# Optimization experiments

Measured on AMD Instinct MI355X. Metric: run time of the kernel, lower is better.

## Reference

```python
import jax, jax.numpy as jnp
import numpy as np

N = 8192      # batch*seq_len (batch=4, seq_len=2048)
DK = 256
DV = 256


def setup_inputs() -> dict:
    key = jax.random.key(0)
    ks = jax.random.split(key, 9)
    s = 1.0 / np.sqrt(DK)
    return {
        "q": jax.random.normal(ks[0], (N, DK), jnp.float32),
        "k": jax.random.normal(ks[1], (N, DK), jnp.float32),
        "v": jax.random.normal(ks[2], (N, DV), jnp.float32),
        "Wq": jax.random.normal(ks[3], (DK, DK), jnp.float32) * s,
        "bq": jnp.zeros((DK,), jnp.float32),
        "Wk": jax.random.normal(ks[4], (DK, DK), jnp.float32) * s,
        "bk": jnp.zeros((DK,), jnp.float32),
        "Wv": jax.random.normal(ks[5], (DV, DV), jnp.float32) * s,
        "bv": jnp.zeros((DV,), jnp.float32),
        "seq_len": 2048,
    }


def reference(q, k, v, Wq, bq, Wk, bk, Wv, bv, seq_len):
    # torch Linear: y = x @ W.T + b
    Q = q @ Wq.T + bq                       # [N, dk]
    K = k @ Wk.T + bk                       # [N, dk]
    V = v @ Wv.T + bv                       # [N, dv]
    sqrt_dk = jnp.sqrt(jnp.asarray(DK, Q.dtype))
    score = (Q @ K.T) / sqrt_dk             # [N, N] — attends over ALL tokens
    # original reshapes to (B, S, N) and softmaxes over dim=-1, which is
    # identical to row-wise softmax on the [N, N] score matrix
    attn = jax.nn.softmax(score, axis=-1)   # [N, N]
    return attn @ V                          # [N, dv]
```

## Files before the change

kernel.cpp:

```cpp
#include <hip/hip_runtime.h>
#include <hip/hip_bf16.h>


typedef __attribute__((ext_vector_type(8))) short short8;
typedef __attribute__((ext_vector_type(4))) short short4v;
typedef __attribute__((ext_vector_type(4))) float f32x4;
typedef __attribute__((ext_vector_type(4))) float float4v;
typedef __attribute__((ext_vector_type(16))) float f32x16;

#define MFMA16 __builtin_amdgcn_mfma_f32_16x16x32_bf16
#define MFMA32 __builtin_amdgcn_mfma_f32_32x32x16_bf16

namespace {
constexpr int kN = 8192;
constexpr int kD = 256;
constexpr int kKVB = 32;
}

__device__ __forceinline__ unsigned short f2bf(float x) {
  union { float f; unsigned u; } v; v.f = x;
  unsigned r = v.u + 0x7FFFu + ((v.u >> 16) & 1u);
  return (unsigned short)(r >> 16);
}

__device__ __forceinline__ unsigned cvtpk_bf16(float lo, float hi) {
  unsigned d;
  asm("v_cvt_pk_bf16_f32 %0, %1, %2" : "=v"(d) : "v"(lo), "v"(hi));
  return d;
}

__device__ __forceinline__ void gll16(const short* g, short* lp) {
  __builtin_amdgcn_global_load_lds(
      (const __attribute__((address_space(1))) void*)g,
      (__attribute__((address_space(3))) void*)lp, 16, 0, 0);
}

__global__ __launch_bounds__(256) void proj_kernel(
    const float* __restrict__ qx, const float* __restrict__ kx, const float* __restrict__ vx,
    const float* __restrict__ Wq, const float* __restrict__ bq,
    const float* __restrict__ Wk, const float* __restrict__ bk,
    const float* __restrict__ Wv, const float* __restrict__ bv,
    short* __restrict__ Qimg, short* __restrict__ Kimg, short* __restrict__ Vimg)
{
  const int mode = blockIdx.z;
  const float* X; const float* W; const float* B;
  if (mode == 0)      { X = qx; W = Wq; B = bq; }
  else if (mode == 1) { X = kx; W = Wk; B = bk; }
  else                { X = vx; W = Wv; B = bv; }

  const int nb = blockIdx.x * 64;
  const int ob = blockIdx.y * 64;

  __shared__ short XA[64][264];
  __shared__ short WB[64][264];

  const int t  = threadIdx.x;
  {
    const int c4 = t & 63;
    const int r0 = t >> 6;
#pragma unroll
    for (int p = 0; p < 16; ++p) {
      const int r = p * 4 + r0;
      float4v xv = *(const float4v*)(X + (size_t)(nb + r) * kD + c4 * 4);
      float4v wv = *(const float4v*)(W + (size_t)(ob + r) * kD + c4 * 4);
      short4v xs, wsv;
#pragma unroll
      for (int j = 0; j < 4; ++j) { xs[j] = (short)f2bf(xv[j]); wsv[j] = (short)f2bf(wv[j]); }
      *(short4v*)(&XA[r][c4 * 4]) = xs;
      *(short4v*)(&WB[r][c4 * 4]) = wsv;
    }
  }
  __syncthreads();

  const int w  = t >> 6;
  const int l  = t & 63;
  const int lr = l & 15;
  const int g  = l >> 4;

  const f32x4 vzero = {0.f, 0.f, 0.f, 0.f};
  f32x4 acc[4];
#pragma unroll
  for (int ct = 0; ct < 4; ++ct) acc[ct] = vzero;

#pragma unroll
  for (int s = 0; s < 8; ++s) {
    short8 af = *(const short8*)(&XA[w * 16 + lr][s * 32 + g * 8]);
#pragma unroll
    for (int ct = 0; ct < 4; ++ct) {
      short8 bf = *(const short8*)(&WB[ct * 16 + lr][s * 32 + g * 8]);
      acc[ct] = MFMA16(af, bf, acc[ct], 0, 0, 0);
    }
  }

#pragma unroll
  for (int ct = 0; ct < 4; ++ct) {
    const int o = ob + ct * 16 + lr;
    const float bias = B[o];
    if (mode == 2) {
      const int n0 = nb + w * 16 + g * 4;
      short4v vs;
#pragma unroll
      for (int r2 = 0; r2 < 4; ++r2) vs[r2] = (short)f2bf(acc[ct][r2] + bias);
      const size_t idx = (size_t)(n0 >> 5) * 8192 + (size_t)(o >> 5) * 1024
                       + (size_t)((n0 >> 4) & 1) * 512 + (size_t)((n0 >> 3) & 1) * 256
                       + (size_t)(o & 31) * 8 + (n0 & 7);
      *(short4v*)(Vimg + idx) = vs;
    } else {
      short* Out = (mode == 0) ? Qimg : Kimg;
      const float sc = (mode == 0) ? 0.0625f : 1.0f;
#pragma unroll
      for (int r2 = 0; r2 < 4; ++r2) {
        const int n = nb + w * 16 + g * 4 + r2;
        const size_t idx = (size_t)(n >> 5) * 8192 + (size_t)(o >> 4) * 512
                         + (size_t)((o >> 3) & 1) * 256 + (size_t)(n & 31) * 8 + (o & 7);
        Out[idx] = (short)f2bf((acc[ct][r2] + bias) * sc);
      }
    }
  }
}

template<int SPLIT>
__global__ __launch_bounds__(512) void flash_kernel(
    const short* __restrict__ Qimg, const short* __restrict__ Kimg, const short* __restrict__ Vimg,
    float* __restrict__ Op, float2* __restrict__ Ml)
{
  constexpr int kIters = (kN / SPLIT) / kKVB;
  const int linear = (int)blockIdx.x;
  int sp, qb;
  if (SPLIT == 8) { sp = linear & 7; qb = linear >> 3; }
  else { const int xcd = linear & 7; sp = xcd >> 1; qb = ((linear >> 3) << 1) | (xcd & 1); }
  const int kvblk0 = sp * (kN / SPLIT / 32);

  __shared__ short sbuf[2][2][8192];

  const int t = threadIdx.x;
  const int w = t >> 6, l = t & 63;
  const int hf = l >> 5;
  const int lc = l & 31;

  {
    const short* kg = Kimg + (size_t)kvblk0 * 8192 + w * 512 + l * 8;
    const short* vg = Vimg + (size_t)kvblk0 * 8192 + w * 512 + l * 8;
    gll16(kg,        &sbuf[0][0][w * 512]);
    gll16(kg + 4096, &sbuf[0][0][4096 + w * 512]);
    gll16(vg,        &sbuf[0][1][w * 512]);
    gll16(vg + 4096, &sbuf[0][1][4096 + w * 512]);
  }

  short8 qf[16];
  {
    const short* qsrc = Qimg + (size_t)(qb * 8 + w) * 8192 + l * 8;
#pragma unroll
    for (int ks = 0; ks < 16; ++ks) qf[ks] = *(const short8*)(qsrc + ks * 512);
  }

  f32x16 oacc[8];
#pragma unroll
  for (int dvt = 0; dvt < 8; ++dvt)
#pragma unroll
    for (int r = 0; r < 16; ++r) oacc[dvt][r] = 0.f;
  float mr = -1e30f, lsum = 0.f;

  asm volatile("s_waitcnt vmcnt(0)" ::: "memory");
  __syncthreads();

  for (int it = 0; it < kIters; ++it) {
    const int cur = it & 1;
    if (it + 1 < kIters) {
      const short* kg = Kimg + (size_t)(kvblk0 + it + 1) * 8192 + w * 512 + l * 8;
      const short* vg = Vimg + (size_t)(kvblk0 + it + 1) * 8192 + w * 512 + l * 8;
      short* kb = &sbuf[cur ^ 1][0][0];
      short* vb = &sbuf[cur ^ 1][1][0];
      gll16(kg,        kb + w * 512);
      gll16(kg + 4096, kb + 4096 + w * 512);
      gll16(vg,        vb + w * 512);
      gll16(vg + 4096, vb + 4096 + w * 512);
    }

    f32x16 sacc;
#pragma unroll
    for (int r = 0; r < 16; ++r) sacc[r] = 0.f;
    __builtin_amdgcn_s_setprio(1);
#pragma unroll
    for (int ks = 0; ks < 16; ++ks) {
      short8 kf = *(const short8*)(&sbuf[cur][0][ks * 512 + l * 8]);
      sacc = MFMA32(kf, qf[ks], sacc, 0, 0, 0);
    }
    __builtin_amdgcn_s_setprio(0);

    float pmax = sacc[0];
#pragma unroll
    for (int r = 1; r < 16; ++r) pmax = fmaxf(pmax, sacc[r]);
    pmax = fmaxf(pmax, __shfl_xor(pmax, 32));
    const bool noskip = !__all(pmax - mr <= 8.f);
    if (noskip) {
      const float newm = fmaxf(mr, pmax);
      const float corr = __expf(mr - newm);
      mr = newm;
      lsum *= corr;
#pragma unroll
      for (int r = 0; r < 16; ++r) {
        const float c = __shfl(corr, (r & 3) + 8 * (r >> 2) + 4 * hf);
#pragma unroll
        for (int dvt = 0; dvt < 8; ++dvt) oacc[dvt][r] *= c;
      }
    }
    float psum = 0.f;
#pragma unroll
    for (int r = 0; r < 16; ++r) { sacc[r] = __expf(sacc[r] - mr); psum += sacc[r]; }
    psum += __shfl_xor(psum, 32);
    lsum += psum;

    short8 pa[2];
#pragma unroll
    for (int w2 = 0; w2 < 2; ++w2) {
      const int b = w2 * 8;
      const unsigned A0 = cvtpk_bf16(sacc[b + 0], sacc[b + 1]);
      const unsigned A1 = cvtpk_bf16(sacc[b + 2], sacc[b + 3]);
      const unsigned B0 = cvtpk_bf16(sacc[b + 4], sacc[b + 5]);
      const unsigned B1 = cvtpk_bf16(sacc[b + 6], sacc[b + 7]);
      const unsigned sA0 = (unsigned)__shfl_xor((int)A0, 32);
      const unsigned sA1 = (unsigned)__shfl_xor((int)A1, 32);
      const unsigned sB0 = (unsigned)__shfl_xor((int)B0, 32);
      const unsigned sB1 = (unsigned)__shfl_xor((int)B1, 32);
      union { unsigned u[4]; short8 s; } pu;
      pu.u[0] = hf ? sB0 : A0;
      pu.u[1] = hf ? sB1 : A1;
      pu.u[2] = hf ? B0 : sA0;
      pu.u[3] = hf ? B1 : sA1;
      pa[w2] = pu.s;
    }

    __builtin_amdgcn_s_setprio(1);
#pragma unroll
    for (int dvt = 0; dvt < 8; ++dvt) {
#pragma unroll
      for (int ks2 = 0; ks2 < 2; ++ks2) {
        short8 vf = *(const short8*)(&sbuf[cur][1][(dvt * 2 + ks2) * 512 + l * 8]);
        oacc[dvt] = MFMA32(pa[ks2], vf, oacc[dvt], 0, 0, 0);
      }
    }
    __builtin_amdgcn_s_setprio(0);

    asm volatile("s_waitcnt vmcnt(0)" ::: "memory");
    __syncthreads();
  }

  const int qrow0 = qb * 256 + w * 32;
#pragma unroll
  for (int dvt = 0; dvt < 8; ++dvt)
#pragma unroll
    for (int r = 0; r < 16; ++r) {
      const int q = qrow0 + (r & 3) + 8 * (r >> 2) + 4 * hf;
      Op[((size_t)sp * kN + q) * kD + dvt * 32 + lc] = oacc[dvt][r];
    }
  if (l < 32) Ml[(size_t)sp * kN + qrow0 + l] = make_float2(mr, lsum);
}

template<int SPLIT>
__global__ __launch_bounds__(256) void merge_kernel(
    const float* __restrict__ Op, const float2* __restrict__ Ml, float* __restrict__ out)
{
  const int qrow = blockIdx.x;
  const int d = threadIdx.x;
  float m[SPLIT], li[SPLIT];
  float M = -1e30f;
#pragma unroll
  for (int s = 0; s < SPLIT; ++s) {
    const float2 a = Ml[(size_t)s * kN + qrow];
    m[s] = a.x; li[s] = a.y;
    M = fmaxf(M, m[s]);
  }
  float L = 0.f, accv = 0.f;
#pragma unroll
  for (int s = 0; s < SPLIT; ++s) {
    const float wgt = __expf(m[s] - M);
    L += wgt * li[s];
    accv += wgt * Op[((size_t)s * kN + qrow) * kD + d];
  }
  out[(size_t)qrow * kD + d] = accv / L;
}

extern "C" void kernel_launch(void* const* d_in, const int* in_sizes, int n_in,
                              void* d_out, int out_size, void* d_ws, size_t ws_size,
                              hipStream_t stream)
{
  const float* q  = (const float*)d_in[0];
  const float* k  = (const float*)d_in[1];
  const float* v  = (const float*)d_in[2];
  const float* Wq = (const float*)d_in[3];
  const float* bq = (const float*)d_in[4];
  const float* Wk = (const float*)d_in[5];
  const float* bk = (const float*)d_in[6];
  const float* Wv = (const float*)d_in[7];
  const float* bv = (const float*)d_in[8];

  char* ws = (char*)d_ws;
  short* Qimg = (short*)(ws);
  short* Kimg = (short*)(ws + ((size_t)4 << 20));
  short* Vimg = (short*)(ws + ((size_t)8 << 20));
  const size_t opOff = (size_t)12 << 20;
  float* Op = (float*)(ws + opOff);

  proj_kernel<<<dim3(kN / 64, kD / 64, 3), 256, 0, stream>>>(
      q, k, v, Wq, bq, Wk, bk, Wv, bv, Qimg, Kimg, Vimg);

  const size_t opBytes8 = (size_t)8 * kN * kD * 4;
  const size_t need8 = opOff + opBytes8 + (size_t)8 * kN * 8;
  if (ws_size >= need8) {
    float2* Ml = (float2*)(ws + opOff + opBytes8);
    flash_kernel<8><<<dim3(256), 512, 0, stream>>>(Qimg, Kimg, Vimg, Op, Ml);
    merge_kernel<8><<<dim3(kN), 256, 0, stream>>>(Op, Ml, (float*)d_out);
  } else {
    const size_t opBytes4 = (size_t)4 * kN * kD * 4;
    float2* Ml = (float2*)(ws + opOff + opBytes4);
    flash_kernel<4><<<dim3(128), 512, 0, stream>>>(Qimg, Kimg, Vimg, Op, Ml);
    merge_kernel<4><<<dim3(kN), 256, 0, stream>>>(Op, Ml, (float*)d_out);
  }
}
```

Before: 112.4 us.

## Shrink flash blocks to 4 waves, reuse X across output tiles, interleave softmax with PV

The flash kernel now runs 256-thread blocks covering 128 query rows, twice as many blocks, with launch bounds requesting two blocks per CU. The KV tile load is restructured to use all 256 threads. The exp/convert/PV path is split into two halves so the second half of the exponentials can overlap the first half's MFMAs. The projection kernel now loads each X tile once and loops over all four W output tiles, and Q/K use a transposed MFMA so their stores become 4-wide vectors. The risks are register pressure under the two-blocks-per-CU bound and a different pattern of KV tile reuse across blocks.

```diff
diff --git a/kernel.cpp b/kernel.cpp
--- a/kernel.cpp
+++ b/kernel.cpp
@@ -35,92 +35,114 @@
       (__attribute__((address_space(3))) void*)lp, 16, 0, 0);
 }
 
-__global__ __launch_bounds__(256) void proj_kernel(
+__global__ __launch_bounds__(256, 2) void proj_kernel(
     const float* __restrict__ qx, const float* __restrict__ kx, const float* __restrict__ vx,
     const float* __restrict__ Wq, const float* __restrict__ bq,
     const float* __restrict__ Wk, const float* __restrict__ bk,
     const float* __restrict__ Wv, const float* __restrict__ bv,
     short* __restrict__ Qimg, short* __restrict__ Kimg, short* __restrict__ Vimg)
 {
-  const int mode = blockIdx.z;
+  const int mode = blockIdx.y;
   const float* X; const float* W; const float* B;
   if (mode == 0)      { X = qx; W = Wq; B = bq; }
   else if (mode == 1) { X = kx; W = Wk; B = bk; }
   else                { X = vx; W = Wv; B = bv; }
 
   const int nb = blockIdx.x * 64;
-  const int ob = blockIdx.y * 64;
 
   __shared__ short XA[64][264];
   __shared__ short WB[64][264];
 
   const int t  = threadIdx.x;
-  {
-    const int c4 = t & 63;
-    const int r0 = t >> 6;
-#pragma unroll
-    for (int p = 0; p < 16; ++p) {
-      const int r = p * 4 + r0;
-      float4v xv = *(const float4v*)(X + (size_t)(nb + r) * kD + c4 * 4);
-      float4v wv = *(const float4v*)(W + (size_t)(ob + r) * kD + c4 * 4);
-      short4v xs, wsv;
-#pragma unroll
-      for (int j = 0; j < 4; ++j) { xs[j] = (short)f2bf(xv[j]); wsv[j] = (short)f2bf(wv[j]); }
-      *(short4v*)(&XA[r][c4 * 4]) = xs;
-      *(short4v*)(&WB[r][c4 * 4]) = wsv;
-    }
-  }
-  __syncthreads();
+  const int c4 = t & 63;
+  const int r0 = t >> 6;
+
+#pragma unroll
+  for (int p = 0; p < 16; ++p) {
+    const int r = p * 4 + r0;
+    float4v xv = *(const float4v*)(X + (size_t)(nb + r) * kD + c4 * 4);
+    short4v xs;
+#pragma unroll
+    for (int j = 0; j < 4; ++j) xs[j] = (short)f2bf(xv[j]);
+    *(short4v*)(&XA[r][c4 * 4]) = xs;
+  }
 
   const int w  = t >> 6;
   const int l  = t & 63;
   const int lr = l & 15;
   const int g  = l >> 4;
 
-  const f32x4 vzero = {0.f, 0.f, 0.f, 0.f};
-  f32x4 acc[4];
-#pragma unroll
-  for (int ct = 0; ct < 4; ++ct) acc[ct] = vzero;
-
-#pragma unroll
-  for (int s = 0; s < 8; ++s) {
-    short8 af = *(const short8*)(&XA[w * 16 + lr][s * 32 + g * 8]);
-#pragma unroll
-    for (int ct = 0; ct < 4; ++ct) {
-      short8 bf = *(const short8*)(&WB[ct * 16 + lr][s * 32 + g * 8]);
-      acc[ct] = MFMA16(af, bf, acc[ct], 0, 0, 0);
-    }
-  }
-
-#pragma unroll
-  for (int ct = 0; ct < 4; ++ct) {
-    const int o = ob + ct * 16 + lr;
-    const float bias = B[o];
+  for (int obi = 0; obi < 4; ++obi) {
+    __syncthreads();
+#pragma unroll
+    for (int p = 0; p < 16; ++p) {
+      const int r = p * 4 + r0;
+      float4v wv = *(const float4v*)(W + (size_t)(obi * 64 + r) * kD + c4 * 4);
+      short4v wsv;
+#pragma unroll
+      for (int j = 0; j < 4; ++j) wsv[j] = (short)f2bf(wv[j]);
+      *(short4v*)(&WB[r][c4 * 4]) = wsv;
+    }
+    __syncthreads();
+
+    const f32x4 vzero = {0.f, 0.f, 0.f, 0.f};
+    f32x4 acc[4];
+#pragma unroll
+    for (int ct = 0; ct < 4; ++ct) acc[ct] = vzero;
+
     if (mode == 2) {
-      const int n0 = nb + w * 16 + g * 4;
-      short4v vs;
-#pragma unroll
-      for (int r2 = 0; r2 < 4; ++r2) vs[r2] = (short)f2bf(acc[ct][r2] + bias);
-      const size_t idx = (size_t)(n0 >> 5) * 8192 + (size_t)(o >> 5) * 1024
-                       + (size_t)((n0 >> 4) & 1) * 512 + (size_t)((n0 >> 3) & 1) * 256
-                       + (size_t)(o & 31) * 8 + (n0 & 7);
-      *(short4v*)(Vimg + idx) = vs;
+#pragma unroll
+      for (int s = 0; s < 8; ++s) {
+        short8 af = *(const short8*)(&XA[w * 16 + lr][s * 32 + g * 8]);
+#pragma unroll
+        for (int ct = 0; ct < 4; ++ct) {
+          short8 bf = *(const short8*)(&WB[ct * 16 + lr][s * 32 + g * 8]);
+          acc[ct] = MFMA16(af, bf, acc[ct], 0, 0, 0);
+        }
+      }
+#pragma unroll
+      for (int ct = 0; ct < 4; ++ct) {
+        const int o = obi * 64 + ct * 16 + lr;
+        const float bias = B[o];
+        const int n0 = nb + w * 16 + g * 4;
+        short4v vs;
+#pragma unroll
+        for (int r2 = 0; r2 < 4; ++r2) vs[r2] = (short)f2bf(acc[ct][r2] + bias);
+        const size_t idx = (size_t)(n0 >> 5) * 8192 + (size_t)(o >> 5) * 1024
+                         + (size_t)((n0 >> 4) & 1) * 512 + (size_t)((n0 >> 3) & 1) * 256
+                         + (size_t)(o & 31) * 8 + (n0 & 7);
+        *(short4v*)(Vimg + idx) = vs;
+      }
     } else {
+#pragma unroll
+      for (int s = 0; s < 8; ++s) {
+        short8 af = *(const short8*)(&WB[w * 16 + lr][s * 32 + g * 8]);
+#pragma unroll
+        for (int ct = 0; ct < 4; ++ct) {
+          short8 bf = *(const short8*)(&XA[ct * 16 + lr][s * 32 + g * 8]);
+          acc[ct] = MFMA16(af, bf, acc[ct], 0, 0, 0);
+        }
+      }
       short* Out = (mode == 0) ? Qimg : Kimg;
       const float sc = (mode == 0) ? 0.0625f : 1.0f;
-#pragma unroll
-      for (int r2 = 0; r2 < 4; ++r2) {
-        const int n = nb + w * 16 + g * 4 + r2;
-        const size_t idx = (size_t)(n >> 5) * 8192 + (size_t)(o >> 4) * 512
-                         + (size_t)((o >> 3) & 1) * 256 + (size_t)(n & 31) * 8 + (o & 7);
-        Out[idx] = (short)f2bf((acc[ct][r2] + bias) * sc);
+      const int o0 = obi * 64 + w * 16 + g * 4;
+      const float4v bv4 = *(const float4v*)(B + o0);
+#pragma unroll
+      for (int ct = 0; ct < 4; ++ct) {
+        const int n = nb + ct * 16 + lr;
+        short4v os;
+#pragma unroll
+        for (int r2 = 0; r2 < 4; ++r2) os[r2] = (short)f2bf((acc[ct][r2] + bv4[r2]) * sc);
+        const size_t idx = (size_t)(n >> 5) * 8192 + (size_t)(o0 >> 4) * 512
+                         + (size_t)((o0 >> 3) & 1) * 256 + (size_t)(n & 31) * 8 + (o0 & 7);
+        *(short4v*)(Out + idx) = os;
       }
     }
   }
 }
 
 template<int SPLIT>
-__global__ __launch_bounds__(512) void flash_kernel(
+__global__ __launch_bounds__(256, 2) void flash_kernel(
     const short* __restrict__ Qimg, const short* __restrict__ Kimg, const short* __restrict__ Vimg,
     float* __restrict__ Op, float2* __restrict__ Ml)
 {
@@ -139,17 +161,18 @@
   const int lc = l & 31;
 
   {
-    const short* kg = Kimg + (size_t)kvblk0 * 8192 + w * 512 + l * 8;
-    const short* vg = Vimg + (size_t)kvblk0 * 8192 + w * 512 + l * 8;
-    gll16(kg,        &sbuf[0][0][w * 512]);
-    gll16(kg + 4096, &sbuf[0][0][4096 + w * 512]);
-    gll16(vg,        &sbuf[0][1][w * 512]);
-    gll16(vg + 4096, &sbuf[0][1][4096 + w * 512]);
+    const short* kg = Kimg + (size_t)kvblk0 * 8192 + t * 8;
+    const short* vg = Vimg + (size_t)kvblk0 * 8192 + t * 8;
+#pragma unroll
+    for (int p = 0; p < 4; ++p) {
+      gll16(kg + p * 2048, &sbuf[0][0][p * 2048 + t * 8]);
+      gll16(vg + p * 2048, &sbuf[0][1][p * 2048 + t * 8]);
+    }
   }
 
   short8 qf[16];
   {
-    const short* qsrc = Qimg + (size_t)(qb * 8 + w) * 8192 + l * 8;
+    const short* qsrc = Qimg + (size_t)(qb * 4 + w) * 8192 + l * 8;
 #pragma unroll
     for (int ks = 0; ks < 16; ++ks) qf[ks] = *(const short8*)(qsrc + ks * 512);
   }
@@ -167,14 +190,15 @@
   for (int it = 0; it < kIters; ++it) {
     const int cur = it & 1;
     if (it + 1 < kIters) {
-      const short* kg = Kimg + (size_t)(kvblk0 + it + 1) * 8192 + w * 512 + l * 8;
-      const short* vg = Vimg + (size_t)(kvblk0 + it + 1) * 8192 + w * 512 + l * 8;
+      const short* kg = Kimg + (size_t)(kvblk0 + it + 1) * 8192 + t * 8;
+      const short* vg = Vimg + (size_t)(kvblk0 + it + 1) * 8192 + t * 8;
       short* kb = &sbuf[cur ^ 1][0][0];
       short* vb = &sbuf[cur ^ 1][1][0];
-      gll16(kg,        kb + w * 512);
-      gll16(kg + 4096, kb + 4096 + w * 512);
-      gll16(vg,        vb + w * 512);
-      gll16(vg + 4096, vb + 4096 + w * 512);
+#pragma unroll
+      for (int p = 0; p < 4; ++p) {
+        gll16(kg + p * 2048, kb + p * 2048 + t * 8);
+        gll16(vg + p * 2048, vb + p * 2048 + t * 8);
+      }
     }
 
     f32x16 sacc;
@@ -192,8 +216,7 @@
 #pragma unroll
     for (int r = 1; r < 16; ++r) pmax = fmaxf(pmax, sacc[r]);
     pmax = fmaxf(pmax, __shfl_xor(pmax, 32));
-    const bool noskip = !__all(pmax - mr <= 8.f);
-    if (noskip) {
+    if (!__all(pmax - mr <= 8.f)) {
       const float newm = fmaxf(mr, pmax);
       const float corr = __expf(mr - newm);
       mr = newm;
@@ -205,20 +228,16 @@
         for (int dvt = 0; dvt < 8; ++dvt) oacc[dvt][r] *= c;
       }
     }
+
     float psum = 0.f;
 #pragma unroll
-    for (int r = 0; r < 16; ++r) { sacc[r] = __expf(sacc[r] - mr); psum += sacc[r]; }
-    psum += __shfl_xor(psum, 32);
-    lsum += psum;
-
-    short8 pa[2];
-#pragma unroll
-    for (int w2 = 0; w2 < 2; ++w2) {
-      const int b = w2 * 8;
-      const unsigned A0 = cvtpk_bf16(sacc[b + 0], sacc[b + 1]);
-      const unsigned A1 = cvtpk_bf16(sacc[b + 2], sacc[b + 3]);
-      const unsigned B0 = cvtpk_bf16(sacc[b + 4], sacc[b + 5]);
-      const unsigned B1 = cvtpk_bf16(sacc[b + 6], sacc[b + 7]);
+    for (int r = 0; r < 8; ++r) { sacc[r] = __expf(sacc[r] - mr); psum += sacc[r]; }
+    short8 pa0;
+    {
+      const unsigned A0 = cvtpk_bf16(sacc[0], sacc[1]);
+      const unsigned A1 = cvtpk_bf16(sacc[2], sacc[3]);
+      const unsigned B0 = cvtpk_bf16(sacc[4], sacc[5]);
+      const unsigned B1 = cvtpk_bf16(sacc[6], sacc[7]);
       const unsigned sA0 = (unsigned)__shfl_xor((int)A0, 32);
       const unsigned sA1 = (unsigned)__shfl_xor((int)A1, 32);
       const unsigned sB0 = (unsigned)__shfl_xor((int)B0, 32);
@@ -228,25 +247,51 @@
       pu.u[1] = hf ? sB1 : A1;
       pu.u[2] = hf ? B0 : sA0;
       pu.u[3] = hf ? B1 : sA1;
-      pa[w2] = pu.s;
-    }
-
+      pa0 = pu.s;
+    }
     __builtin_amdgcn_s_setprio(1);
 #pragma unroll
     for (int dvt = 0; dvt < 8; ++dvt) {
-#pragma unroll
-      for (int ks2 = 0; ks2 < 2; ++ks2) {
-        short8 vf = *(const short8*)(&sbuf[cur][1][(dvt * 2 + ks2) * 512 + l * 8]);
-        oacc[dvt] = MFMA32(pa[ks2], vf, oacc[dvt], 0, 0, 0);
-      }
+      short8 vf = *(const short8*)(&sbuf[cur][1][(dvt * 2) * 512 + l * 8]);
+      oacc[dvt] = MFMA32(pa0, vf, oacc[dvt], 0, 0, 0);
     }
     __builtin_amdgcn_s_setprio(0);
+
+#pragma unroll
+    for (int r = 8; r < 16; ++r) { sacc[r] = __expf(sacc[r] - mr); psum += sacc[r]; }
+    short8 pa1;
+    {
+      const unsigned A0 = cvtpk_bf16(sacc[8], sacc[9]);
+      const unsigned A1 = cvtpk_bf16(sacc[10], sacc[11]);
+      const unsigned B0 = cvtpk_bf16(sacc[12], sacc[13]);
+      const unsigned B1 = cvtpk_bf16(sacc[14], sacc[15]);
+      const unsigned sA0 = (unsigned)__shfl_xor((int)A0, 32);
+      const unsigned sA1 = (unsigned)__shfl_xor((int)A1, 32);
+      const unsigned sB0 = (unsigned)__shfl_xor((int)B0, 32);
+      const unsigned sB1 = (unsigned)__shfl_xor((int)B1, 32);
+      union { unsigned u[4]; short8 s; } pu;
+      pu.u[0] = hf ? sB0 : A0;
+      pu.u[1] = hf ? sB1 : A1;
+      pu.u[2] = hf ? B0 : sA0;
+      pu.u[3] = hf ? B1 : sA1;
+      pa1 = pu.s;
+    }
+    __builtin_amdgcn_s_setprio(1);
+#pragma unroll
+    for (int dvt = 0; dvt < 8; ++dvt) {
+      short8 vf = *(const short8*)(&sbuf[cur][1][(dvt * 2 + 1) * 512 + l * 8]);
+      oacc[dvt] = MFMA32(pa1, vf, oacc[dvt], 0, 0, 0);
+    }
+    __builtin_amdgcn_s_setprio(0);
+
+    psum += __shfl_xor(psum, 32);
+    lsum += psum;
 
     asm volatile("s_waitcnt vmcnt(0)" ::: "memory");
     __syncthreads();
   }
 
-  const int qrow0 = qb * 256 + w * 32;
+  const int qrow0 = qb * 128 + w * 32;
 #pragma unroll
   for (int dvt = 0; dvt < 8; ++dvt)
 #pragma unroll
@@ -302,19 +347,19 @@
   const size_t opOff = (size_t)12 << 20;
   float* Op = (float*)(ws + opOff);
 
-  proj_kernel<<<dim3(kN / 64, kD / 64, 3), 256, 0, stream>>>(
+  proj_kernel<<<dim3(kN / 64, 3), 256, 0, stream>>>(
       q, k, v, Wq, bq, Wk, bk, Wv, bv, Qimg, Kimg, Vimg);
 
   const size_t opBytes8 = (size_t)8 * kN * kD * 4;
   const size_t need8 = opOff + opBytes8 + (size_t)8 * kN * 8;
   if (ws_size >= need8) {
     float2* Ml = (float2*)(ws + opOff + opBytes8);
-    flash_kernel<8><<<dim3(256), 512, 0, stream>>>(Qimg, Kimg, Vimg, Op, Ml);
+    flash_kernel<8><<<dim3(512), 256, 0, stream>>>(Qimg, Kimg, Vimg, Op, Ml);
     merge_kernel<8><<<dim3(kN), 256, 0, stream>>>(Op, Ml, (float*)d_out);
   } else {
     const size_t opBytes4 = (size_t)4 * kN * kD * 4;
     float2* Ml = (float2*)(ws + opOff + opBytes4);
-    flash_kernel<4><<<dim3(128), 512, 0, stream>>>(Qimg, Kimg, Vimg, Op, Ml);
+    flash_kernel<4><<<dim3(256), 256, 0, stream>>>(Qimg, Kimg, Vimg, Op, Ml);
     merge_kernel<4><<<dim3(kN), 256, 0, stream>>>(Op, Ml, (float*)d_out);
   }
 }
```

After: 115.0 us. 1.02x slower.
